# Kernel optimization log

Measured on AMD Instinct MI355X. Metric: run time of the kernel, lower is better.

Reference implementation:

```python
import jax, jax.numpy as jnp
import numpy as np

EPS = 1e-12  # clamp for sqrt stability in Gram-matrix distance

def _pairwise_euclid(X, Y):
    # [B,D],[M,D] -> [B,M] Euclidean distances via Gram trick (avoids [B,M,D] diff tensor)
    x2 = jnp.sum(X * X, axis=-1, keepdims=True)        # [B,1]
    y2 = jnp.sum(Y * Y, axis=-1)[None, :]              # [1,M]
    sq = x2 + y2 - 2.0 * (X @ Y.T)
    return jnp.sqrt(jnp.maximum(sq, EPS))

def setup_inputs() -> dict:
    key = jax.random.key(0)
    k1, k2, k3 = jax.random.split(key, 3)
    B, D = 4096, 128
    return {
        "rep_anchor": jax.random.normal(k1, (B, D), dtype=jnp.float32),
        "rep_pos": jax.random.normal(k2, (B, D), dtype=jnp.float32),
        "rep_neg": jax.random.normal(k3, (B, D), dtype=jnp.float32),
    }

def reference(rep_anchor, rep_pos, rep_neg):
    B = rep_anchor.shape[0]
    # distance_pos[i] = ||a_i - p_i||_2 (elementwise rows, like F.pairwise_distance)
    diff = rep_anchor - rep_pos
    distance_pos = jnp.sqrt(jnp.maximum(jnp.sum(diff * diff, axis=-1), EPS))  # [B]

    big = jnp.asarray(jnp.finfo(rep_anchor.dtype).max, rep_anchor.dtype)
    eye = jnp.eye(B, dtype=bool)
    # anchor-as-negative: exclude self (index i)
    d_aa = jnp.where(eye, big, _pairwise_euclid(rep_anchor, rep_anchor))  # [B,B]
    # pos-as-negative: rep_pos[i] is excluded for anchor i
    d_ap = jnp.where(eye, big, _pairwise_euclid(rep_anchor, rep_pos))    # [B,B]
    # all of rep_neg are negatives
    d_an = _pairwise_euclid(rep_anchor, rep_neg)                          # [B,B]

    hardest_neg = jnp.minimum(jnp.minimum(d_aa.min(axis=1), d_ap.min(axis=1)), d_an.min(axis=1))  # [B]
    # log1p(exp(x)) == softplus, computed stably
    loss_in_batch = jnp.logaddexp(0.0, distance_pos - hardest_neg)
    return jnp.mean(loss_in_batch)
```

## Files before the change

### kernel.cpp

```cpp
#include <hip/hip_runtime.h>
#include <math.h>

#define BDIM 4096
#define DDIM 128
#define EPSF 1e-12f
#define TI 128
#define TJ 64
#define NSPLIT 16
#define NSLICE (NSPLIT * 2)
#define ITILES (BDIM / TI)
#define JT 12
#define FLT_BIG 3.402823466e+38f
#define MATSZ (BDIM * DDIM)
#define YBUF (TJ * DDIM)

typedef __attribute__((ext_vector_type(8))) _Float16 f16x8;
typedef __attribute__((ext_vector_type(16))) float f32x16;

__device__ __forceinline__ void gload_lds16(const void* g, void* l) {
    __builtin_amdgcn_global_load_lds(
        (const __attribute__((address_space(1))) unsigned int*)(uintptr_t)g,
        (__attribute__((address_space(3))) unsigned int*)(unsigned int)(uintptr_t)l,
        16, 0, 0);
}

__device__ __forceinline__ unsigned int pack2h(float x, float y) {
    _Float16 hx = (_Float16)x, hy = (_Float16)y;
    unsigned short ux, uy;
    __builtin_memcpy(&ux, &hx, 2);
    __builtin_memcpy(&uy, &hy, 2);
    return (unsigned int)ux | ((unsigned int)uy << 16);
}

__global__ __launch_bounds__(256) void prep_kernel(
    const float* __restrict__ A, const float* __restrict__ P,
    const float* __restrict__ N, ushort* __restrict__ Xf,
    float* __restrict__ a2, float* __restrict__ p2,
    float* __restrict__ n2, float* __restrict__ dpos) {
    int row = (blockIdx.x * blockDim.x + threadIdx.x) >> 6;
    int lane = threadIdx.x & 63;
    if (row >= BDIM) return;
    const float2 av = *(const float2*)&A[row * DDIM + lane * 2];
    const float2 pv = *(const float2*)&P[row * DDIM + lane * 2];
    const float2 nv = *(const float2*)&N[row * DDIM + lane * 2];
    *(unsigned int*)&Xf[0 * MATSZ + row * DDIM + lane * 2] = pack2h(av.x, av.y);
    *(unsigned int*)&Xf[1 * MATSZ + row * DDIM + lane * 2] = pack2h(pv.x, pv.y);
    *(unsigned int*)&Xf[2 * MATSZ + row * DDIM + lane * 2] = pack2h(nv.x, nv.y);
    float sa = av.x * av.x + av.y * av.y;
    float sp = pv.x * pv.x + pv.y * pv.y;
    float sn = nv.x * nv.x + nv.y * nv.y;
    float dx = av.x - pv.x, dy = av.y - pv.y;
    float sd = dx * dx + dy * dy;
    #pragma unroll
    for (int off = 32; off; off >>= 1) {
        sa += __shfl_down(sa, off);
        sp += __shfl_down(sp, off);
        sn += __shfl_down(sn, off);
        sd += __shfl_down(sd, off);
    }
    if (lane == 0) {
        a2[row] = sa;
        p2[row] = sp;
        n2[row] = sn;
        dpos[row] = sqrtf(fmaxf(sd, EPSF));
    }
}

__device__ __forceinline__ void stage_Y(const ushort* g, int j0, ushort* dst,
                                        int w, int lane) {
    int sub = lane >> 4;
    int s = lane & 15;
    #pragma unroll
    for (int q = 0; q < 4; ++q) {
        int r = w * 16 + q * 4 + sub;
        int sp = s ^ (r & 15);
        gload_lds16(g + (size_t)(j0 + r) * DDIM + sp * 8,
                    dst + (w * 16 + q * 4) * DDIM);
    }
}

__global__ __launch_bounds__(256, 2) void minsq_kernel(
    const ushort* __restrict__ Xf,
    const float* __restrict__ a2, const float* __restrict__ p2,
    const float* __restrict__ n2, float* __restrict__ partial) {
    __shared__ __align__(16) ushort pool[4][YBUF];
    ushort* const base = &pool[0][0];

    const int tid = threadIdx.x;
    const int w = tid >> 6;
    const int lane = tid & 63;
    const int rg = w >> 1;
    const int ch = w & 1;
    const int iTile = blockIdx.x;
    const int split = blockIdx.y;
    const int i0 = iTile * TI;
    const int jt0 = split * JT;
    const int sub = lane >> 4, s = lane & 15;

    #pragma unroll
    for (int q = 0; q < 8; ++q) {
        int r = w * 32 + q * 4 + sub;
        int sp = s ^ (r & 15);
        gload_lds16(Xf + (size_t)(i0 + r) * DDIM + sp * 8,
                    base + (w * 32 + q * 4) * DDIM);
    }
    stage_Y(Xf + (size_t)(jt0 >> 6) * MATSZ, (jt0 & 63) * TJ, base + 2 * YBUF, w, lane);
    stage_Y(Xf + (size_t)((jt0 + 1) >> 6) * MATSZ, ((jt0 + 1) & 63) * TJ,
            base + 3 * YBUF, w, lane);

    asm volatile("s_waitcnt vmcnt(8)" ::: "memory");
    __builtin_amdgcn_s_barrier();
    __builtin_amdgcn_sched_barrier(0);

    f16x8 afr[2][8];
    #pragma unroll
    for (int rb = 0; rb < 2; ++rb) {
        int r = rg * 64 + rb * 32 + (lane & 31);
        #pragma unroll
        for (int t = 0; t < 8; ++t) {
            int sl = t * 2 + (lane >> 5);
            int sp = sl ^ (r & 15);
            afr[rb][t] = *(const f16x8*)&base[r * DDIM + sp * 8];
        }
    }
    float y2h[JT];
    #pragma unroll
    for (int t = 0; t < JT; ++t) {
        int jt = jt0 + t, m = jt >> 6, tc = jt & 63;
        const float* y2g = (m == 0) ? a2 : ((m == 1) ? p2 : n2);
        y2h[t] = 0.5f * y2g[tc * TJ + ch * 32 + (lane & 31)];
    }
    asm volatile("s_waitcnt lgkmcnt(0)" ::: "memory");
    __builtin_amdgcn_sched_barrier(0);
    __builtin_amdgcn_s_barrier();
    __builtin_amdgcn_sched_barrier(0);

    float minv[2][16];
    #pragma unroll
    for (int rb = 0; rb < 2; ++rb)
        #pragma unroll
        for (int g = 0; g < 16; ++g) minv[rb][g] = FLT_BIG;

    #pragma unroll
    for (int idx = 0; idx < JT; ++idx) {
        if (idx + 2 < JT) {
            int jn = jt0 + idx + 2;
            stage_Y(Xf + (size_t)(jn >> 6) * MATSZ, (jn & 63) * TJ,
                    base + (idx & 3) * YBUF, w, lane);
        }
        if (idx < JT - 2)       asm volatile("s_waitcnt vmcnt(8)" ::: "memory");
        else if (idx == JT - 2) asm volatile("s_waitcnt vmcnt(4)" ::: "memory");
        else                    asm volatile("s_waitcnt vmcnt(0)" ::: "memory");
        __builtin_amdgcn_s_barrier();
        __builtin_amdgcn_sched_barrier(0);

        const ushort* bufY = base + ((idx + 2) & 3) * YBUF;
        f32x16 acc0 = {};
        f32x16 acc1 = {};
        {
            int r = ch * 32 + (lane & 31);
            __builtin_amdgcn_s_setprio(1);
            #pragma unroll
            for (int t = 0; t < 8; ++t) {
                int sl = t * 2 + (lane >> 5);
                int sp = sl ^ (r & 15);
                f16x8 b = *(const f16x8*)&bufY[r * DDIM + sp * 8];
                acc0 = __builtin_amdgcn_mfma_f32_32x32x16_f16(afr[0][t], b, acc0, 0, 0, 0);
                acc1 = __builtin_amdgcn_mfma_f32_32x32x16_f16(afr[1][t], b, acc1, 0, 0, 0);
            }
            __builtin_amdgcn_s_setprio(0);
        }

        {
            int jt = jt0 + idx, m = jt >> 6, tc = jt & 63;
            float yh = y2h[idx];
            if (m < 2 && (tc >> 1) == iTile) {
                int jg = tc * TJ + ch * 32 + (lane & 31);
                #pragma unroll
                for (int rb = 0; rb < 2; ++rb) {
                    #pragma unroll
                    for (int g = 0; g < 16; ++g) {
                        int rloc = (g & 3) + 8 * (g >> 2) + 4 * (lane >> 5);
                        int ig = i0 + rg * 64 + rb * 32 + rloc;
                        float d = (rb == 0) ? acc0[g] : acc1[g];
                        float cand = yh - d;
                        if (ig == jg) cand = FLT_BIG;
                        minv[rb][g] = fminf(minv[rb][g], cand);
                    }
                }
            } else {
                #pragma unroll
                for (int g = 0; g < 16; ++g) {
                    minv[0][g] = fminf(minv[0][g], yh - acc0[g]);
                    minv[1][g] = fminf(minv[1][g], yh - acc1[g]);
                }
            }
        }
    }

    #pragma unroll
    for (int off = 1; off < 32; off <<= 1) {
        #pragma unroll
        for (int rb = 0; rb < 2; ++rb)
            #pragma unroll
            for (int g = 0; g < 16; ++g)
                minv[rb][g] = fminf(minv[rb][g], __shfl_xor(minv[rb][g], off));
    }
    if ((lane & 31) == 0) {
        int hi = lane >> 5;
        int slice = split * 2 + ch;
        #pragma unroll
        for (int rb = 0; rb < 2; ++rb) {
            #pragma unroll
            for (int g = 0; g < 16; ++g) {
                int rloc = (g & 3) + 8 * (g >> 2) + 4 * hi;
                int ig = i0 + rg * 64 + rb * 32 + rloc;
                partial[(size_t)ig * NSLICE + slice] = minv[rb][g];
            }
        }
    }
}

__global__ __launch_bounds__(256) void lossA_kernel(
    const float* __restrict__ partial, const float* __restrict__ a2,
    const float* __restrict__ dpos, float* __restrict__ bsum) {
    __shared__ float red[4];
    int i = blockIdx.x * 256 + threadIdx.x;
    const float4* pr = (const float4*)&partial[(size_t)i * NSLICE];
    float mv = FLT_BIG;
    #pragma unroll
    for (int q = 0; q < NSLICE / 4; ++q) {
        float4 v = pr[q];
        mv = fminf(mv, fminf(fminf(v.x, v.y), fminf(v.z, v.w)));
    }
    float h2 = a2[i] + 2.0f * mv;
    float hardest = sqrtf(fmaxf(h2, EPSF));
    float x = dpos[i] - hardest;
    float sum = fmaxf(x, 0.f) + log1pf(expf(-fabsf(x)));
    #pragma unroll
    for (int off = 32; off; off >>= 1) sum += __shfl_down(sum, off);
    if ((threadIdx.x & 63) == 0) red[threadIdx.x >> 6] = sum;
    __syncthreads();
    if (threadIdx.x == 0)
        bsum[blockIdx.x] = red[0] + red[1] + red[2] + red[3];
}

__global__ void lossB_kernel(const float* __restrict__ bsum,
                             float* __restrict__ out) {
    float v = (threadIdx.x < 16) ? bsum[threadIdx.x] : 0.f;
    #pragma unroll
    for (int off = 32; off; off >>= 1) v += __shfl_down(v, off);
    if (threadIdx.x == 0) out[0] = v * (1.0f / BDIM);
}

extern "C" void kernel_launch(void* const* d_in, const int* in_sizes, int n_in,
                              void* d_out, int out_size, void* d_ws, size_t ws_size,
                              hipStream_t stream) {
    const float* A = (const float*)d_in[0];
    const float* P = (const float*)d_in[1];
    const float* N = (const float*)d_in[2];

    float* ws = (float*)d_ws;
    float* a2 = ws;
    float* p2 = ws + BDIM;
    float* n2 = ws + 2 * BDIM;
    float* dpos = ws + 3 * BDIM;
    float* bsum = ws + 4 * BDIM;
    float* partial = ws + 4 * BDIM + 64;
    ushort* Xf = (ushort*)(partial + (size_t)NSLICE * BDIM);

    prep_kernel<<<BDIM / 4, 256, 0, stream>>>(A, P, N, Xf, a2, p2, n2, dpos);
    dim3 grid2(ITILES, NSPLIT);
    minsq_kernel<<<grid2, 256, 0, stream>>>(Xf, a2, p2, n2, partial);
    lossA_kernel<<<16, 256, 0, stream>>>(partial, a2, dpos, bsum);
    lossB_kernel<<<1, 64, 0, stream>>>(bsum, (float*)d_out);
}
```

Baseline: 35.58 us.

## Widen Y tile to 128 columns with 2x2 MFMA blocking and double buffering

Doubles the Y tile width per iteration to 128 columns, so each wave computes a 2x2 grid of 32x32 MFMA blocks and reuses both the A and B fragments. The A fragments now load straight from global memory into registers instead of being staged through LDS. The four-deep LDS ring is replaced by a double buffer with one extra barrier per iteration. This halves the loop trip count and the barriers per unit of work, in exchange for more accumulator registers (four f32x16) and a shallower prefetch pipeline.

```diff
diff --git a/kernel.cpp b/kernel.cpp
--- a/kernel.cpp
+++ b/kernel.cpp
@@ -5,14 +5,14 @@
 #define DDIM 128
 #define EPSF 1e-12f
 #define TI 128
-#define TJ 64
+#define TJc 128
 #define NSPLIT 16
 #define NSLICE (NSPLIT * 2)
 #define ITILES (BDIM / TI)
-#define JT 12
+#define JT 6
 #define FLT_BIG 3.402823466e+38f
 #define MATSZ (BDIM * DDIM)
-#define YBUF (TJ * DDIM)
+#define YBUF (TJc * DDIM)
 
 typedef __attribute__((ext_vector_type(8))) _Float16 f16x8;
 typedef __attribute__((ext_vector_type(16))) float f32x16;
@@ -66,25 +66,11 @@
     }
 }
 
-__device__ __forceinline__ void stage_Y(const ushort* g, int j0, ushort* dst,
-                                        int w, int lane) {
-    int sub = lane >> 4;
-    int s = lane & 15;
-    #pragma unroll
-    for (int q = 0; q < 4; ++q) {
-        int r = w * 16 + q * 4 + sub;
-        int sp = s ^ (r & 15);
-        gload_lds16(g + (size_t)(j0 + r) * DDIM + sp * 8,
-                    dst + (w * 16 + q * 4) * DDIM);
-    }
-}
-
 __global__ __launch_bounds__(256, 2) void minsq_kernel(
     const ushort* __restrict__ Xf,
     const float* __restrict__ a2, const float* __restrict__ p2,
     const float* __restrict__ n2, float* __restrict__ partial) {
-    __shared__ __align__(16) ushort pool[4][YBUF];
-    ushort* const base = &pool[0][0];
+    __shared__ __align__(16) ushort Y[2][YBUF];
 
     const int tid = threadIdx.x;
     const int w = tid >> 6;
@@ -97,126 +83,128 @@
     const int jt0 = split * JT;
     const int sub = lane >> 4, s = lane & 15;
 
-    #pragma unroll
-    for (int q = 0; q < 8; ++q) {
-        int r = w * 32 + q * 4 + sub;
-        int sp = s ^ (r & 15);
-        gload_lds16(Xf + (size_t)(i0 + r) * DDIM + sp * 8,
-                    base + (w * 32 + q * 4) * DDIM);
-    }
-    stage_Y(Xf + (size_t)(jt0 >> 6) * MATSZ, (jt0 & 63) * TJ, base + 2 * YBUF, w, lane);
-    stage_Y(Xf + (size_t)((jt0 + 1) >> 6) * MATSZ, ((jt0 + 1) & 63) * TJ,
-            base + 3 * YBUF, w, lane);
-
-    asm volatile("s_waitcnt vmcnt(8)" ::: "memory");
-    __builtin_amdgcn_s_barrier();
-    __builtin_amdgcn_sched_barrier(0);
-
-    f16x8 afr[2][8];
-    #pragma unroll
-    for (int rb = 0; rb < 2; ++rb) {
-        int r = rg * 64 + rb * 32 + (lane & 31);
+    {
+        int m = jt0 >> 5, tc = jt0 & 31;
+        const ushort* g = Xf + (size_t)m * MATSZ + (size_t)tc * TJc * DDIM;
+        #pragma unroll
+        for (int q = 0; q < 8; ++q) {
+            int r = w * 32 + q * 4 + sub;
+            int sp = s ^ (r & 15);
+            gload_lds16(g + (size_t)r * DDIM + sp * 8,
+                        &Y[0][(w * 32 + q * 4) * DDIM]);
+        }
+    }
+    f16x8 a0[8], a1[8];
+    {
+        const ushort* r0 = Xf + (size_t)(i0 + rg * 64 + (lane & 31)) * DDIM;
+        const ushort* r1 = r0 + 32 * DDIM;
         #pragma unroll
         for (int t = 0; t < 8; ++t) {
             int sl = t * 2 + (lane >> 5);
-            int sp = sl ^ (r & 15);
-            afr[rb][t] = *(const f16x8*)&base[r * DDIM + sp * 8];
-        }
-    }
-    float y2h[JT];
+            a0[t] = *(const f16x8*)(r0 + sl * 8);
+            a1[t] = *(const f16x8*)(r1 + sl * 8);
+        }
+    }
+    float y2h0[JT], y2h1[JT];
     #pragma unroll
     for (int t = 0; t < JT; ++t) {
-        int jt = jt0 + t, m = jt >> 6, tc = jt & 63;
+        int jt = jt0 + t, m = jt >> 5, tc = jt & 31;
         const float* y2g = (m == 0) ? a2 : ((m == 1) ? p2 : n2);
-        y2h[t] = 0.5f * y2g[tc * TJ + ch * 32 + (lane & 31)];
-    }
-    asm volatile("s_waitcnt lgkmcnt(0)" ::: "memory");
-    __builtin_amdgcn_sched_barrier(0);
-    __builtin_amdgcn_s_barrier();
-    __builtin_amdgcn_sched_barrier(0);
-
-    float minv[2][16];
-    #pragma unroll
-    for (int rb = 0; rb < 2; ++rb)
-        #pragma unroll
-        for (int g = 0; g < 16; ++g) minv[rb][g] = FLT_BIG;
+        int jb = tc * TJc + ch * 64 + (lane & 31);
+        y2h0[t] = 0.5f * y2g[jb];
+        y2h1[t] = 0.5f * y2g[jb + 32];
+    }
+
+    float minv0[16], minv1[16];
+    #pragma unroll
+    for (int g = 0; g < 16; ++g) { minv0[g] = FLT_BIG; minv1[g] = FLT_BIG; }
 
     #pragma unroll
     for (int idx = 0; idx < JT; ++idx) {
-        if (idx + 2 < JT) {
-            int jn = jt0 + idx + 2;
-            stage_Y(Xf + (size_t)(jn >> 6) * MATSZ, (jn & 63) * TJ,
-                    base + (idx & 3) * YBUF, w, lane);
-        }
-        if (idx < JT - 2)       asm volatile("s_waitcnt vmcnt(8)" ::: "memory");
-        else if (idx == JT - 2) asm volatile("s_waitcnt vmcnt(4)" ::: "memory");
-        else                    asm volatile("s_waitcnt vmcnt(0)" ::: "memory");
+        if (idx + 1 < JT) {
+            int jn = jt0 + idx + 1, m = jn >> 5, tc = jn & 31;
+            const ushort* g = Xf + (size_t)m * MATSZ + (size_t)tc * TJc * DDIM;
+            #pragma unroll
+            for (int q = 0; q < 8; ++q) {
+                int r = w * 32 + q * 4 + sub;
+                int sp = s ^ (r & 15);
+                gload_lds16(g + (size_t)r * DDIM + sp * 8,
+                            &Y[(idx + 1) & 1][(w * 32 + q * 4) * DDIM]);
+            }
+            asm volatile("s_waitcnt vmcnt(8)" ::: "memory");
+        } else {
+            asm volatile("s_waitcnt vmcnt(0)" ::: "memory");
+        }
+        __builtin_amdgcn_sched_barrier(0);
         __builtin_amdgcn_s_barrier();
         __builtin_amdgcn_sched_barrier(0);
 
-        const ushort* bufY = base + ((idx + 2) & 3) * YBUF;
-        f32x16 acc0 = {};
-        f32x16 acc1 = {};
+        const ushort* buf = &Y[idx & 1][0];
+        const int rB0 = ch * 64 + (lane & 31);
+        const int rB1 = rB0 + 32;
+        f32x16 acc00 = {}, acc01 = {}, acc10 = {}, acc11 = {};
+        __builtin_amdgcn_s_setprio(1);
+        #pragma unroll
+        for (int t = 0; t < 8; ++t) {
+            int sl = t * 2 + (lane >> 5);
+            f16x8 b0 = *(const f16x8*)&buf[rB0 * DDIM + (sl ^ (rB0 & 15)) * 8];
+            f16x8 b1 = *(const f16x8*)&buf[rB1 * DDIM + (sl ^ (rB1 & 15)) * 8];
+            acc00 = __builtin_amdgcn_mfma_f32_32x32x16_f16(a0[t], b0, acc00, 0, 0, 0);
+            acc10 = __builtin_amdgcn_mfma_f32_32x32x16_f16(a1[t], b0, acc10, 0, 0, 0);
+            acc01 = __builtin_amdgcn_mfma_f32_32x32x16_f16(a0[t], b1, acc01, 0, 0, 0);
+            acc11 = __builtin_amdgcn_mfma_f32_32x32x16_f16(a1[t], b1, acc11, 0, 0, 0);
+        }
+        __builtin_amdgcn_s_setprio(0);
+
         {
-            int r = ch * 32 + (lane & 31);
-            __builtin_amdgcn_s_setprio(1);
-            #pragma unroll
-            for (int t = 0; t < 8; ++t) {
-                int sl = t * 2 + (lane >> 5);
-                int sp = sl ^ (r & 15);
-                f16x8 b = *(const f16x8*)&bufY[r * DDIM + sp * 8];
-                acc0 = __builtin_amdgcn_mfma_f32_32x32x16_f16(afr[0][t], b, acc0, 0, 0, 0);
-                acc1 = __builtin_amdgcn_mfma_f32_32x32x16_f16(afr[1][t], b, acc1, 0, 0, 0);
-            }
-            __builtin_amdgcn_s_setprio(0);
-        }
-
-        {
-            int jt = jt0 + idx, m = jt >> 6, tc = jt & 63;
-            float yh = y2h[idx];
-            if (m < 2 && (tc >> 1) == iTile) {
-                int jg = tc * TJ + ch * 32 + (lane & 31);
+            int jt = jt0 + idx, m = jt >> 5, tc = jt & 31;
+            float yh0 = y2h0[idx], yh1 = y2h1[idx];
+            if (m < 2 && tc == iTile) {
+                int jg0 = tc * TJc + ch * 64 + (lane & 31);
+                int jg1 = jg0 + 32;
                 #pragma unroll
-                for (int rb = 0; rb < 2; ++rb) {
-                    #pragma unroll
-                    for (int g = 0; g < 16; ++g) {
-                        int rloc = (g & 3) + 8 * (g >> 2) + 4 * (lane >> 5);
-                        int ig = i0 + rg * 64 + rb * 32 + rloc;
-                        float d = (rb == 0) ? acc0[g] : acc1[g];
-                        float cand = yh - d;
-                        if (ig == jg) cand = FLT_BIG;
-                        minv[rb][g] = fminf(minv[rb][g], cand);
-                    }
+                for (int g = 0; g < 16; ++g) {
+                    int rloc = (g & 3) + 8 * (g >> 2) + 4 * (lane >> 5);
+                    int ig0 = i0 + rg * 64 + rloc;
+                    int ig1 = ig0 + 32;
+                    float c;
+                    c = yh0 - acc00[g]; if (ig0 == jg0) c = FLT_BIG;
+                    minv0[g] = fminf(minv0[g], c);
+                    c = yh1 - acc01[g]; if (ig0 == jg1) c = FLT_BIG;
+                    minv0[g] = fminf(minv0[g], c);
+                    c = yh0 - acc10[g]; if (ig1 == jg0) c = FLT_BIG;
+                    minv1[g] = fminf(minv1[g], c);
+                    c = yh1 - acc11[g]; if (ig1 == jg1) c = FLT_BIG;
+                    minv1[g] = fminf(minv1[g], c);
                 }
             } else {
                 #pragma unroll
                 for (int g = 0; g < 16; ++g) {
-                    minv[0][g] = fminf(minv[0][g], yh - acc0[g]);
-                    minv[1][g] = fminf(minv[1][g], yh - acc1[g]);
+                    minv0[g] = fminf(minv0[g], fminf(yh0 - acc00[g], yh1 - acc01[g]));
+                    minv1[g] = fminf(minv1[g], fminf(yh0 - acc10[g], yh1 - acc11[g]));
                 }
             }
         }
+        __builtin_amdgcn_s_barrier();
     }
 
     #pragma unroll
     for (int off = 1; off < 32; off <<= 1) {
         #pragma unroll
-        for (int rb = 0; rb < 2; ++rb)
-            #pragma unroll
-            for (int g = 0; g < 16; ++g)
-                minv[rb][g] = fminf(minv[rb][g], __shfl_xor(minv[rb][g], off));
+        for (int g = 0; g < 16; ++g) {
+            minv0[g] = fminf(minv0[g], __shfl_xor(minv0[g], off));
+            minv1[g] = fminf(minv1[g], __shfl_xor(minv1[g], off));
+        }
     }
     if ((lane & 31) == 0) {
         int hi = lane >> 5;
         int slice = split * 2 + ch;
         #pragma unroll
-        for (int rb = 0; rb < 2; ++rb) {
-            #pragma unroll
-            for (int g = 0; g < 16; ++g) {
-                int rloc = (g & 3) + 8 * (g >> 2) + 4 * hi;
-                int ig = i0 + rg * 64 + rb * 32 + rloc;
-                partial[(size_t)ig * NSLICE + slice] = minv[rb][g];
-            }
+        for (int g = 0; g < 16; ++g) {
+            int rloc = (g & 3) + 8 * (g >> 2) + 4 * hi;
+            int ig = i0 + rg * 64 + rloc;
+            partial[(size_t)ig * NSLICE + slice] = minv0[g];
+            partial[(size_t)(ig + 32) * NSLICE + slice] = minv1[g];
         }
     }
 }
@@ -267,7 +255,7 @@
     float* dpos = ws + 3 * BDIM;
     float* bsum = ws + 4 * BDIM;
     float* partial = ws + 4 * BDIM + 64;
-    ushort* Xf = (ushort*)(partial + (size_t)NSLICE * BDIM);
+    ushort* Xf = (ushort*)(partial + (size_t)BDIM * NSLICE);
 
     prep_kernel<<<BDIM / 4, 256, 0, stream>>>(A, P, N, Xf, a2, p2, n2, dpos);
     dim3 grid2(ITILES, NSPLIT);
```

After: 38.37 us. 1.08x slower.

## Load A fragments directly from global, triple-buffer Y, double the j-split

Applied to the files above, without the earlier changes.

The kernel now loads the A-row fragments straight from global memory into registers instead of staging them through LDS, which shrinks shared memory to three Y buffers. The pipeline moves from 4-buffer prefetch-depth-2 to 3-buffer prefetch-depth-1. NSPLIT doubles and JT halves, giving more blocks with shorter loops, and launch bounds rise to 3 blocks per SM. The goal is higher occupancy and more parallelism, at the cost of a shallower prefetch and uncoalesced strided global loads for A.

```diff
diff --git a/kernel.cpp b/kernel.cpp
--- a/kernel.cpp
+++ b/kernel.cpp
@@ -6,13 +6,12 @@
 #define EPSF 1e-12f
 #define TI 128
 #define TJ 64
-#define NSPLIT 16
+#define NSPLIT 32
 #define NSLICE (NSPLIT * 2)
 #define ITILES (BDIM / TI)
-#define JT 12
+#define JT 6
 #define FLT_BIG 3.402823466e+38f
 #define MATSZ (BDIM * DDIM)
-#define YBUF (TJ * DDIM)
 
 typedef __attribute__((ext_vector_type(8))) _Float16 f16x8;
 typedef __attribute__((ext_vector_type(16))) float f32x16;
@@ -79,12 +78,11 @@
     }
 }
 
-__global__ __launch_bounds__(256, 2) void minsq_kernel(
+__global__ __launch_bounds__(256, 3) void minsq_kernel(
     const ushort* __restrict__ Xf,
     const float* __restrict__ a2, const float* __restrict__ p2,
     const float* __restrict__ n2, float* __restrict__ partial) {
-    __shared__ __align__(16) ushort pool[4][YBUF];
-    ushort* const base = &pool[0][0];
+    __shared__ __align__(16) ushort Y[3][TJ * DDIM];
 
     const int tid = threadIdx.x;
     const int w = tid >> 6;
@@ -95,32 +93,18 @@
     const int split = blockIdx.y;
     const int i0 = iTile * TI;
     const int jt0 = split * JT;
-    const int sub = lane >> 4, s = lane & 15;
-
-    #pragma unroll
-    for (int q = 0; q < 8; ++q) {
-        int r = w * 32 + q * 4 + sub;
-        int sp = s ^ (r & 15);
-        gload_lds16(Xf + (size_t)(i0 + r) * DDIM + sp * 8,
-                    base + (w * 32 + q * 4) * DDIM);
-    }
-    stage_Y(Xf + (size_t)(jt0 >> 6) * MATSZ, (jt0 & 63) * TJ, base + 2 * YBUF, w, lane);
-    stage_Y(Xf + (size_t)((jt0 + 1) >> 6) * MATSZ, ((jt0 + 1) & 63) * TJ,
-            base + 3 * YBUF, w, lane);
-
-    asm volatile("s_waitcnt vmcnt(8)" ::: "memory");
-    __builtin_amdgcn_s_barrier();
-    __builtin_amdgcn_sched_barrier(0);
-
-    f16x8 afr[2][8];
-    #pragma unroll
-    for (int rb = 0; rb < 2; ++rb) {
-        int r = rg * 64 + rb * 32 + (lane & 31);
+
+    stage_Y(Xf + (size_t)(jt0 >> 6) * MATSZ, (jt0 & 63) * TJ, Y[0], w, lane);
+
+    f16x8 a0[8], a1[8];
+    {
+        const ushort* r0 =
+            Xf + (size_t)(i0 + rg * 64 + (lane & 31)) * DDIM + (lane >> 5) * 8;
+        const ushort* r1 = r0 + 32 * DDIM;
         #pragma unroll
         for (int t = 0; t < 8; ++t) {
-            int sl = t * 2 + (lane >> 5);
-            int sp = sl ^ (r & 15);
-            afr[rb][t] = *(const f16x8*)&base[r * DDIM + sp * 8];
+            a0[t] = *(const f16x8*)(r0 + t * 16);
+            a1[t] = *(const f16x8*)(r1 + t * 16);
         }
     }
     float y2h[JT];
@@ -130,10 +114,6 @@
         const float* y2g = (m == 0) ? a2 : ((m == 1) ? p2 : n2);
         y2h[t] = 0.5f * y2g[tc * TJ + ch * 32 + (lane & 31)];
     }
-    asm volatile("s_waitcnt lgkmcnt(0)" ::: "memory");
-    __builtin_amdgcn_sched_barrier(0);
-    __builtin_amdgcn_s_barrier();
-    __builtin_amdgcn_sched_barrier(0);
 
     float minv[2][16];
     #pragma unroll
@@ -142,38 +122,35 @@
         for (int g = 0; g < 16; ++g) minv[rb][g] = FLT_BIG;
 
     #pragma unroll
-    for (int idx = 0; idx < JT; ++idx) {
-        if (idx + 2 < JT) {
-            int jn = jt0 + idx + 2;
+    for (int t = 0; t < JT; ++t) {
+        if (t + 1 < JT) {
+            int jn = jt0 + t + 1;
             stage_Y(Xf + (size_t)(jn >> 6) * MATSZ, (jn & 63) * TJ,
-                    base + (idx & 3) * YBUF, w, lane);
-        }
-        if (idx < JT - 2)       asm volatile("s_waitcnt vmcnt(8)" ::: "memory");
-        else if (idx == JT - 2) asm volatile("s_waitcnt vmcnt(4)" ::: "memory");
-        else                    asm volatile("s_waitcnt vmcnt(0)" ::: "memory");
+                    Y[(t + 1) % 3], w, lane);
+            asm volatile("s_waitcnt vmcnt(4)" ::: "memory");
+        } else {
+            asm volatile("s_waitcnt vmcnt(0)" ::: "memory");
+        }
+        __builtin_amdgcn_sched_barrier(0);
         __builtin_amdgcn_s_barrier();
         __builtin_amdgcn_sched_barrier(0);
 
-        const ushort* bufY = base + ((idx + 2) & 3) * YBUF;
-        f32x16 acc0 = {};
-        f32x16 acc1 = {};
+        const ushort* buf = Y[t % 3];
+        const int rB = ch * 32 + (lane & 31);
+        f32x16 acc0 = {}, acc1 = {};
+        __builtin_amdgcn_s_setprio(1);
+        #pragma unroll
+        for (int k = 0; k < 8; ++k) {
+            int sl = k * 2 + (lane >> 5);
+            f16x8 b = *(const f16x8*)&buf[rB * DDIM + (sl ^ (rB & 15)) * 8];
+            acc0 = __builtin_amdgcn_mfma_f32_32x32x16_f16(a0[k], b, acc0, 0, 0, 0);
+            acc1 = __builtin_amdgcn_mfma_f32_32x32x16_f16(a1[k], b, acc1, 0, 0, 0);
+        }
+        __builtin_amdgcn_s_setprio(0);
+
         {
-            int r = ch * 32 + (lane & 31);
-            __builtin_amdgcn_s_setprio(1);
-            #pragma unroll
-            for (int t = 0; t < 8; ++t) {
-                int sl = t * 2 + (lane >> 5);
-                int sp = sl ^ (r & 15);
-                f16x8 b = *(const f16x8*)&bufY[r * DDIM + sp * 8];
-                acc0 = __builtin_amdgcn_mfma_f32_32x32x16_f16(afr[0][t], b, acc0, 0, 0, 0);
-                acc1 = __builtin_amdgcn_mfma_f32_32x32x16_f16(afr[1][t], b, acc1, 0, 0, 0);
-            }
-            __builtin_amdgcn_s_setprio(0);
-        }
-
-        {
-            int jt = jt0 + idx, m = jt >> 6, tc = jt & 63;
-            float yh = y2h[idx];
+            int jt = jt0 + t, m = jt >> 6, tc = jt & 63;
+            float yh = y2h[t];
             if (m < 2 && (tc >> 1) == iTile) {
                 int jg = tc * TJ + ch * 32 + (lane & 31);
                 #pragma unroll
@@ -267,7 +244,7 @@
     float* dpos = ws + 3 * BDIM;
     float* bsum = ws + 4 * BDIM;
     float* partial = ws + 4 * BDIM + 64;
-    ushort* Xf = (ushort*)(partial + (size_t)NSLICE * BDIM);
+    ushort* Xf = (ushort*)(partial + (size_t)BDIM * NSLICE);
 
     prep_kernel<<<BDIM / 4, 256, 0, stream>>>(A, P, N, Xf, a2, p2, n2, dpos);
     dim3 grid2(ITILES, NSPLIT);
```

Result: slower. 91.26 us (+156.5%).
